# Kernel optimization log

Hardware: AMD Instinct MI355X
Metric: run time of the kernel (lower is better)

## Reference

```python
import jax, jax.numpy as jnp
import numpy as np

H = 2048          # hidden_size
NH = 32           # num_attention_heads
NKV = 8           # num_key_value_heads
HD = H // NH      # head_dim = 64
GROUPS = NH // NKV
B, S = 1, 4096


def setup_inputs() -> dict:
    key = jax.random.key(0)
    k1, k2, k3, k4, k5 = jax.random.split(key, 5)
    hidden_states = jax.random.normal(k1, (B, S, H), dtype=jnp.float32)
    # additive causal mask [B, 1, S, S]
    causal = jnp.tril(jnp.ones((S, S), dtype=bool))
    attention_mask = jnp.where(causal, 0.0, jnp.finfo(jnp.float32).min)[None, None].astype(jnp.float32)
    scale = 0.02
    Wq = jax.random.normal(k2, (H, H), dtype=jnp.float32) * scale
    Wk = jax.random.normal(k3, (NKV * HD, H), dtype=jnp.float32) * scale
    Wv = jax.random.normal(k4, (NKV * HD, H), dtype=jnp.float32) * scale
    Wo = jax.random.normal(k5, (H, H), dtype=jnp.float32) * scale
    return {"hidden_states": hidden_states, "attention_mask": attention_mask,
            "Wq": Wq, "Wk": Wk, "Wv": Wv, "Wo": Wo}


def reference(hidden_states, attention_mask, Wq, Wk, Wv, Wo):
    bsz, q_len, _ = hidden_states.shape
    # projections (nn.Linear: x @ W.T)
    q = (hidden_states @ Wq.T).reshape(bsz, q_len, NH, HD).transpose(0, 2, 1, 3)   # [B,NH,S,HD]
    k = (hidden_states @ Wk.T).reshape(bsz, q_len, NKV, HD).transpose(0, 2, 1, 3)  # [B,NKV,S,HD]
    v = (hidden_states @ Wv.T).reshape(bsz, q_len, NKV, HD).transpose(0, 2, 1, 3)
    # repeat_kv: expand each KV head GROUPS times
    k = jnp.repeat(k, GROUPS, axis=1)  # [B,NH,S,HD]
    v = jnp.repeat(v, GROUPS, axis=1)
    attn_weights = jnp.einsum('bhqd,bhkd->bhqk', q, k) / jnp.sqrt(jnp.float32(HD))
    attn_weights = attn_weights + attention_mask
    attn_weights = jax.nn.softmax(attn_weights.astype(jnp.float32), axis=-1).astype(q.dtype)
    attn_output = jnp.einsum('bhqk,bhkd->bhqd', attn_weights, v)
    attn_output = attn_output.transpose(0, 2, 1, 3).reshape(bsz, q_len, H)
    return attn_output @ Wo.T
```

## Files before the change

### kernel.cpp

```cpp
#include <hip/hip_runtime.h>
#include <stdint.h>

#define S_LEN  4096
#define HDIM   2048
#define NHEADS 32
#define NKVH   8
#define HDSZ   64
#define KVDIM  (NKVH * HDSZ)
#define QKN    (HDIM + KVDIM)

typedef __bf16 v8bf16 __attribute__((ext_vector_type(8)));
typedef short  v4s    __attribute__((ext_vector_type(4)));
typedef float  v4f32  __attribute__((ext_vector_type(4)));

__device__ __forceinline__ unsigned short f2bf(float f) {
    uint32_t u = __builtin_bit_cast(uint32_t, f);
    uint32_t r = (u + 0x7fffu + ((u >> 16) & 1u)) >> 16;
    return (unsigned short)r;
}

__device__ __forceinline__ uint32_t pack_bf16(float a, float b) {
#if __has_builtin(__builtin_amdgcn_cvt_pk_bf16_f32)
    auto r = __builtin_amdgcn_cvt_pk_bf16_f32(a, b);
    return __builtin_bit_cast(uint32_t, r);
#else
    uint32_t ua = __builtin_bit_cast(uint32_t, a) + 0x8000u;
    uint32_t ub = __builtin_bit_cast(uint32_t, b) + 0x8000u;
    return (ua >> 16) | (ub & 0xffff0000u);
#endif
}

__device__ __forceinline__ float fast_exp2(float x) {
#if __has_builtin(__builtin_amdgcn_exp2f)
    return __builtin_amdgcn_exp2f(x);
#else
    float r; asm("v_exp_f32 %0, %1" : "=v"(r) : "v"(x)); return r;
#endif
}

__device__ __forceinline__ void async_load16(const void* g, void* l) {
    __builtin_amdgcn_global_load_lds((const __attribute__((address_space(1))) void*)g,
                                     (__attribute__((address_space(3))) void*)l,
                                     16, 0, 0);
}

#define SEG0 2097152
#define SEG1 3145728
#define SEG2 3407872
#define SEG3 3670016
#define SEGT 4718592
__global__ void cvt_all(const float* __restrict__ x,  const float* __restrict__ wq,
                        const float* __restrict__ wk, const float* __restrict__ wv,
                        const float* __restrict__ wo,
                        ushort4* __restrict__ xb, ushort4* __restrict__ wqkb,
                        ushort4* __restrict__ wvb, ushort4* __restrict__ wob,
                        float qscale)
{
    int i = blockIdx.x * blockDim.x + threadIdx.x;
    if (i >= SEGT) return;
    const float4* src; ushort4* dst; float s = 1.0f; int loc;
    if (i < SEG0)      { src = (const float4*)x;  dst = xb;   loc = i; }
    else if (i < SEG1) { src = (const float4*)wq; dst = wqkb; loc = i - SEG0; s = qscale; }
    else if (i < SEG2) { src = (const float4*)wk; dst = wqkb + 1048576; loc = i - SEG1; }
    else if (i < SEG3) { src = (const float4*)wv; dst = wvb;  loc = i - SEG2; }
    else               { src = (const float4*)wo; dst = wob;  loc = i - SEG3; }
    float4 f = src[loc];
    uint2 o;
    o.x = pack_bf16(f.x * s, f.y * s);
    o.y = pack_bf16(f.z * s, f.w * s);
    dst[loc] = __builtin_bit_cast(ushort4, o);
}


#define STAGE_A(buf, kh, t)                                                       \
    do {                                                                          \
        async_load16(A + aBase + (size_t)(t) * 64 + (kh) * 32,                    \
                     &smem[(buf) * 16384 + (kh) * 8192 + ldsSt]);                 \
        async_load16(A + aBase + (size_t)128 * Kd + (size_t)(t) * 64 + (kh) * 32, \
                     &smem[(buf) * 16384 + (kh) * 8192 + ldsSt + 4096]);          \
    } while (0)
#define STAGE_B(buf, kh, t)                                                       \
    do {                                                                          \
        async_load16(Bp + bBase + (size_t)(t) * 64 + (kh) * 32,                   \
                     &smem[32768 + (buf) * 16384 + (kh) * 8192 + ldsSt]);         \
        async_load16(Bp + bBase + (size_t)128 * Kd + (size_t)(t) * 64 + (kh) * 32,\
                     &smem[32768 + (buf) * 16384 + (kh) * 8192 + ldsSt + 4096]);  \
    } while (0)

#define LOAD_AF(khoff)                                                            \
    do {                                                                          \
        _Pragma("unroll")                                                         \
        for (int mi = 0; mi < 8; ++mi)                                            \
            af[mi] = *(const v8bf16*)&smem[curA + (khoff) + aRd + mi * 512];      \
    } while (0)

#define MFMA_PAIR(khoff, NI)                                                      \
    do {                                                                          \
        v8bf16 _b0 = *(const v8bf16*)&smem[curB + (khoff) + bRd + (NI) * 512];    \
        v8bf16 _b1 = *(const v8bf16*)&smem[curB + (khoff) + bRd + (NI) * 512 + 512];\
        __builtin_amdgcn_s_setprio(1);                                            \
        _Pragma("unroll")                                                         \
        for (int mi = 0; mi < 8; ++mi) {                                          \
            acc[mi][(NI)]     = __builtin_amdgcn_mfma_f32_16x16x32_bf16(af[mi], _b0, acc[mi][(NI)], 0, 0, 0);     \
            acc[mi][(NI) + 1] = __builtin_amdgcn_mfma_f32_16x16x32_bf16(af[mi], _b1, acc[mi][(NI) + 1], 0, 0, 0); \
        }                                                                         \
        __builtin_amdgcn_s_setprio(0);                                            \
    } while (0)

#define FENCE_BAR()                                                               \
    do {                                                                          \
        __builtin_amdgcn_sched_barrier(0);                                        \
        __builtin_amdgcn_s_barrier();                                             \
        __builtin_amdgcn_sched_barrier(0);                                        \
    } while (0)

#define WAITV(N) asm volatile("s_waitcnt vmcnt(" #N ")" ::: "memory")

template<bool F32OUT>
__device__ __forceinline__ void gemm256_body(
    const unsigned short* __restrict__ A,
    const unsigned short* __restrict__ Bp,
    void* __restrict__ Cout, int Nn, int Kd, int m0, int n0,
    unsigned short* __restrict__ smem)
{
    const int tid  = threadIdx.x;
    const int wave = tid >> 6;
    const int lane = tid & 63;
    const int lrow = lane & 15;
    const int quad = lane >> 4;
    const int wm = (wave >> 2) * 128;
    const int wn = (wave & 3) * 64;

    const int lr   = lane >> 2;
    const int sg4  = (lane & 3) ^ ((lane >> 3) & 3);
    const size_t aBase = (size_t)(m0 + wave * 16 + lr) * Kd + sg4 * 8;
    const size_t bBase = (size_t)(n0 + wave * 16 + lr) * Kd + sg4 * 8;
    const int ldsSt = wave * 512;

    const int rg4 = (quad ^ ((lrow >> 1) & 3)) * 8;
    const int aRd = (wm + lrow) * 32 + rg4;
    const int bRd = (wn + lrow) * 32 + rg4;

    const int NT = Kd >> 6;

    v4f32 acc[8][4];
#pragma unroll
    for (int mi = 0; mi < 8; ++mi)
#pragma unroll
        for (int ni = 0; ni < 4; ++ni)
#pragma unroll
            for (int r = 0; r < 4; ++r) acc[mi][ni][r] = 0.0f;

    STAGE_A(0, 0, 0); STAGE_B(0, 0, 0);
    STAGE_A(0, 1, 0); STAGE_B(0, 1, 0);
    STAGE_A(1, 0, 1); STAGE_B(1, 0, 1);
    WAITV(8);
    __builtin_amdgcn_s_barrier();
    __builtin_amdgcn_sched_barrier(0);

    v8bf16 af[8];
    for (int t = 0; t < NT - 2; ++t) {
        const int cur  = t & 1;
        const int nxt  = cur ^ 1;
        const int curA = cur * 16384;
        const int curB = 32768 + cur * 16384;

        STAGE_A(nxt, 1, t + 1);
        LOAD_AF(0);
        MFMA_PAIR(0, 0);
        FENCE_BAR();

        STAGE_B(nxt, 1, t + 1);
        MFMA_PAIR(0, 2);
        WAITV(8);
        FENCE_BAR();

        STAGE_A(cur, 0, t + 2);
        LOAD_AF(8192);
        MFMA_PAIR(8192, 0);
        FENCE_BAR();

        STAGE_B(cur, 0, t + 2);
        MFMA_PAIR(8192, 2);
        WAITV(8);
        FENCE_BAR();
    }

    {
        const int t = NT - 2;
        const int cur  = t & 1;
        const int nxt  = cur ^ 1;
        const int curA = cur * 16384;
        const int curB = 32768 + cur * 16384;

        STAGE_A(nxt, 1, t + 1);
        LOAD_AF(0);
        MFMA_PAIR(0, 0);
        FENCE_BAR();

        STAGE_B(nxt, 1, t + 1);
        MFMA_PAIR(0, 2);
        WAITV(8);
        FENCE_BAR();

        LOAD_AF(8192);
        MFMA_PAIR(8192, 0);
        FENCE_BAR();

        MFMA_PAIR(8192, 2);
        WAITV(4);
        FENCE_BAR();
    }

    {
        const int cur  = (NT - 1) & 1;
        const int curA = cur * 16384;
        const int curB = 32768 + cur * 16384;

        LOAD_AF(0);
        MFMA_PAIR(0, 0);
        FENCE_BAR();

        MFMA_PAIR(0, 2);
        WAITV(0);
        FENCE_BAR();

        LOAD_AF(8192);
        MFMA_PAIR(8192, 0);
        FENCE_BAR();

        MFMA_PAIR(8192, 2);
    }

    if (F32OUT) {
        float* Cf = (float*)Cout;
#pragma unroll
        for (int mi = 0; mi < 8; ++mi)
#pragma unroll
            for (int ni = 0; ni < 4; ++ni)
#pragma unroll
                for (int r = 0; r < 4; ++r) {
                    const int row = m0 + wm + mi * 16 + quad * 4 + r;
                    const int col = n0 + wn + ni * 16 + lrow;
                    Cf[(size_t)row * Nn + col] = acc[mi][ni][r];
                }
    } else {
        unsigned short* Cb = (unsigned short*)Cout;
#pragma unroll
        for (int mi = 0; mi < 8; ++mi)
#pragma unroll
            for (int ni = 0; ni < 4; ++ni)
#pragma unroll
                for (int r = 0; r < 4; ++r) {
                    const int row = m0 + wm + mi * 16 + quad * 4 + r;
                    const int col = n0 + wn + ni * 16 + lrow;
                    Cb[(size_t)row * Nn + col] = f2bf(acc[mi][ni][r]);
                }
    }
}

__global__ __launch_bounds__(512, 2)
void gemm_qkv256(const unsigned short* __restrict__ xb,
                 const unsigned short* __restrict__ Wqkb,
                 const unsigned short* __restrict__ Wvb,
                 unsigned short* __restrict__ QKb,
                 unsigned short* __restrict__ Vtb)
{
    __shared__ __align__(16) unsigned short smem[65536];
    const int bid = blockIdx.x;
    if (bid < 32) {
        gemm256_body<false>(Wvb, xb, Vtb, S_LEN, HDIM,
                            (bid >> 4) * 256, (bid & 15) * 256, smem);
    } else {
        const int b = bid - 32;
        gemm256_body<false>(xb, Wqkb, QKb, QKN, HDIM,
                            (b & 15) * 256, (b >> 4) * 256, smem);
    }
}

__global__ __launch_bounds__(512, 2)
void gemm_o256(const unsigned short* __restrict__ A,
               const unsigned short* __restrict__ B,
               float* __restrict__ Cout)
{
    __shared__ __align__(16) unsigned short smem[65536];
    const int bid = blockIdx.x;
    gemm256_body<true>(A, B, Cout, HDIM, HDIM,
                       (bid & 15) * 256, (bid >> 4) * 256, smem);
}

__global__ __launch_bounds__(256, 3)
void flash_attn(const unsigned short* __restrict__ QK,
                const unsigned short* __restrict__ Vt,
                unsigned short* __restrict__ O)
{
    __shared__ unsigned short smem[24576];
    unsigned short* Qs = smem;

    const int tid  = threadIdx.x;
    const int wave = tid >> 6;
    const int lane = tid & 63;
    const int lrow = lane & 15;
    const int quad = lane >> 4;

    const int h   = blockIdx.x;
    const int kvh = h >> 2;
    const int q0  = (gridDim.y - 1 - blockIdx.y) * 128;

    const int srow8 = lane >> 3;
    const int sgrp  = (lane & 7) ^ srow8;
    const v8bf16 v_one8 = __builtin_bit_cast(v8bf16,
        (uint4){0x3F803F80u, 0x3F803F80u, 0x3F803F80u, 0x3F803F80u});

    {
        const size_t gq = (size_t)(q0 + wave * 32 + srow8) * QKN + h * HDSZ + sgrp * 8;
#pragma unroll
        for (int i = 0; i < 4; ++i)
            async_load16(QK + gq + (size_t)(i * 8) * QKN, &Qs[(wave * 32 + i * 8) * 64]);
    }

    int kperm[2];
#pragma unroll
    for (int i = 0; i < 2; ++i) {
        const int slot = wave * 16 + i * 8 + srow8;
        const int nj = slot >> 4, sm = slot & 15;
        kperm[i] = 32 * (nj >> 1) + 8 * (sm >> 2) + 4 * (nj & 1) + (sm & 3);
    }

    auto stage_kv = [&](int j) {
        const int k0b = j * 64;
        const int buf = (j & 1) * 4096;
#pragma unroll
        for (int i = 0; i < 2; ++i) {
            const size_t gk = (size_t)(k0b + kperm[i]) * QKN
                              + HDIM + kvh * HDSZ + sgrp * 8;
            async_load16(QK + gk, &smem[8192 + buf + (wave * 16 + i * 8) * 64]);
        }
        const size_t gv = (size_t)(kvh * HDSZ + wave * 16 + srow8) * S_LEN
                          + k0b + sgrp * 8;
        async_load16(Vt + gv,             &smem[16384 + buf + (wave * 16) * 64]);
        async_load16(Vt + gv + 8 * S_LEN, &smem[16384 + buf + (wave * 16 + 8) * 64]);
    };

    v4f32 o_acc[2][4], l_acc[2];
#pragma unroll
    for (int mi = 0; mi < 2; ++mi) {
#pragma unroll
        for (int r = 0; r < 4; ++r) l_acc[mi][r] = 0.0f;
#pragma unroll
        for (int dj = 0; dj < 4; ++dj)
#pragma unroll
            for (int r = 0; r < 4; ++r) o_acc[mi][dj][r] = 0.0f;
    }

    const int rbase = q0 + wave * 32;
    const int njt   = (q0 >> 6) + 2;

    stage_kv(0);

    for (int j = 0; j < njt; ++j) {
        const int k0  = j * 64;
        const int buf = (j & 1) * 4096;

        if (j + 1 < njt) { stage_kv(j + 1); WAITV(4); }
        else             { WAITV(0); }
        __builtin_amdgcn_sched_barrier(0);
        __builtin_amdgcn_s_barrier();
        __builtin_amdgcn_sched_barrier(0);

        if (k0 <= rbase + 31) {
            const unsigned short* Ks = &smem[8192 + buf];
            const unsigned short* Vs = &smem[16384 + buf];

            v4f32 st[2][4];
#pragma unroll
            for (int mi = 0; mi < 2; ++mi)
#pragma unroll
                for (int nj = 0; nj < 4; ++nj)
#pragma unroll
                    for (int r = 0; r < 4; ++r) st[mi][nj][r] = 0.0f;
#pragma unroll
            for (int kk = 0; kk < 2; ++kk) {
                const int swz = ((kk * 4 + quad) ^ (lrow & 7)) * 8;
                v8bf16 qa[2];
                qa[0] = *(const v8bf16*)&Qs[(wave * 32 + lrow) * 64 + swz];
                qa[1] = *(const v8bf16*)&Qs[(wave * 32 + 16 + lrow) * 64 + swz];
                __builtin_amdgcn_s_setprio(1);
#pragma unroll
                for (int nj = 0; nj < 4; ++nj) {
                    const v8bf16 kb = *(const v8bf16*)&Ks[(nj * 16 + lrow) * 64 + swz];
                    st[0][nj] = __builtin_amdgcn_mfma_f32_16x16x32_bf16(kb, qa[0], st[0][nj], 0, 0, 0);
                    st[1][nj] = __builtin_amdgcn_mfma_f32_16x16x32_bf16(kb, qa[1], st[1][nj], 0, 0, 0);
                }
                __builtin_amdgcn_s_setprio(0);
            }

            if (k0 + 63 > rbase) {
#pragma unroll
                for (int mi = 0; mi < 2; ++mi) {
                    const int qi = rbase + mi * 16 + lrow;
#pragma unroll
                    for (int nj = 0; nj < 4; ++nj) {
                        const int kib = k0 + 32 * (nj >> 1) + 8 * quad + 4 * (nj & 1);
#pragma unroll
                        for (int r = 0; r < 4; ++r)
                            if (kib + r > qi) st[mi][nj][r] = -1e30f;
                    }
                }
            }

            v8bf16 pk8[2][2];
#pragma unroll
            for (int mi = 0; mi < 2; ++mi) {
                uint2 pu[4];
#pragma unroll
                for (int nj = 0; nj < 4; ++nj) {
                    const float p0 = fast_exp2(st[mi][nj][0]);
                    const float p1 = fast_exp2(st[mi][nj][1]);
                    const float p2 = fast_exp2(st[mi][nj][2]);
                    const float p3 = fast_exp2(st[mi][nj][3]);
                    pu[nj].x = pack_bf16(p0, p1);
                    pu[nj].y = pack_bf16(p2, p3);
                }
                pk8[mi][0] = __builtin_bit_cast(v8bf16, (uint4){pu[0].x, pu[0].y, pu[1].x, pu[1].y});
                pk8[mi][1] = __builtin_bit_cast(v8bf16, (uint4){pu[2].x, pu[2].y, pu[3].x, pu[3].y});
            }

#pragma unroll
            for (int t = 0; t < 2; ++t) {
                const int swzv = ((t * 4 + quad) ^ (lrow & 7)) * 8;
                v8bf16 va[4];
#pragma unroll
                for (int dj = 0; dj < 4; ++dj)
                    va[dj] = *(const v8bf16*)&Vs[(dj * 16 + lrow) * 64 + swzv];
                __builtin_amdgcn_s_setprio(1);
#pragma unroll
                for (int dj = 0; dj < 4; ++dj) {
                    o_acc[0][dj] = __builtin_amdgcn_mfma_f32_16x16x32_bf16(va[dj], pk8[0][t], o_acc[0][dj], 0, 0, 0);
                    o_acc[1][dj] = __builtin_amdgcn_mfma_f32_16x16x32_bf16(va[dj], pk8[1][t], o_acc[1][dj], 0, 0, 0);
                }
                l_acc[0] = __builtin_amdgcn_mfma_f32_16x16x32_bf16(v_one8, pk8[0][t], l_acc[0], 0, 0, 0);
                l_acc[1] = __builtin_amdgcn_mfma_f32_16x16x32_bf16(v_one8, pk8[1][t], l_acc[1], 0, 0, 0);
                __builtin_amdgcn_s_setprio(0);
            }
        }

        __builtin_amdgcn_sched_barrier(0);
        __builtin_amdgcn_s_barrier();
        __builtin_amdgcn_sched_barrier(0);
    }

    __syncthreads();
    unsigned short* Os = smem;
#pragma unroll
    for (int mi = 0; mi < 2; ++mi) {
        const float inv = 1.0f / l_acc[mi][0];
#pragma unroll
        for (int dj = 0; dj < 4; ++dj)
#pragma unroll
            for (int r = 0; r < 4; ++r)
                Os[(wave * 32 + mi * 16 + lrow) * 72 + dj * 16 + quad * 4 + r] =
                    f2bf(o_acc[mi][dj][r] * inv);
    }
    __syncthreads();
#pragma unroll
    for (int i = 0; i < 4; ++i) {
        const int idx = i * 256 + tid;
        const int row = idx >> 3, c8 = idx & 7;
        const uint4 vv = *(const uint4*)&Os[row * 72 + c8 * 8];
        *(uint4*)&O[(size_t)(q0 + row) * HDIM + h * HDSZ + c8 * 8] = vv;
    }
}

extern "C" void kernel_launch(void* const* d_in, const int* in_sizes, int n_in,
                              void* d_out, int out_size, void* d_ws, size_t ws_size,
                              hipStream_t stream)
{
    const float* x  = (const float*)d_in[0];
    const float* Wq = (const float*)d_in[2];
    const float* Wk = (const float*)d_in[3];
    const float* Wv = (const float*)d_in[4];
    const float* Wo = (const float*)d_in[5];
    float* out = (float*)d_out;

    unsigned short* xb   = (unsigned short*)d_ws;
    unsigned short* Wqkb = xb   + (size_t)S_LEN * HDIM;
    unsigned short* Wvb  = Wqkb + (size_t)QKN * HDIM;
    unsigned short* Wob  = Wvb  + (size_t)KVDIM * HDIM;
    unsigned short* QKb  = Wob  + (size_t)HDIM * HDIM;
    unsigned short* Vtb  = QKb  + (size_t)S_LEN * QKN;
    unsigned short* AOb  = xb;

    cvt_all<<<(SEGT + 255) / 256, 256, 0, stream>>>(
        x, Wq, Wk, Wv, Wo,
        (ushort4*)xb, (ushort4*)Wqkb, (ushort4*)Wvb, (ushort4*)Wob,
        0.18033688011f);

    gemm_qkv256<<<192, 512, 0, stream>>>(xb, Wqkb, Wvb, QKb, Vtb);

    flash_attn<<<dim3(NHEADS, S_LEN / 128), 256, 0, stream>>>(QKb, Vtb, AOb);

    gemm_o256<<<128, 512, 0, stream>>>(AOb, Wob, out);
}
```

Baseline: 341.7 us.

## Replace O-projection GEMM with 128x256 tile kernel using deeper async pipeline

Swaps the generic 256x256 output-projection GEMM for a dedicated 128x256 tile kernel launched on 256 blocks instead of 128. The new kernel stages the K dimension in 32-wide half-tiles across double buffers, interleaving async global-to-LDS loads with MFMA pairs, and raises wave priority around the MFMAs. The aim is better CU coverage on MI355X, since 128 blocks leave many of its CUs idle, and better overlap of loads with compute. In exchange the tiles are smaller so data reuse per block drops, occupancy is limited to one block per CU, and the kernel carries hand-written prologue and epilogue code.

```diff
diff --git a/kernel.cpp b/kernel.cpp
--- a/kernel.cpp
+++ b/kernel.cpp
@@ -278,15 +278,166 @@
     }
 }
 
-__global__ __launch_bounds__(512, 2)
-void gemm_o256(const unsigned short* __restrict__ A,
-               const unsigned short* __restrict__ B,
+
+#define STAGE2_A(buf, kh, t)                                                      \
+    async_load16(A + aBase + (size_t)(t) * 64 + (kh) * 32,                        \
+                 &smem[(buf) * 8192 + (kh) * 4096 + ldsSt])
+#define STAGE2_B(buf, kh, t)                                                      \
+    do {                                                                          \
+        async_load16(Bp + bBase + (size_t)(t) * 64 + (kh) * 32,                   \
+                     &smem[16384 + (buf) * 16384 + (kh) * 8192 + ldsSt]);         \
+        async_load16(Bp + bBase + (size_t)128 * 2048 + (size_t)(t) * 64 + (kh) * 32,\
+                     &smem[16384 + (buf) * 16384 + (kh) * 8192 + ldsSt + 4096]);  \
+    } while (0)
+
+#define LOAD_AF2(khoff)                                                           \
+    do {                                                                          \
+        _Pragma("unroll")                                                         \
+        for (int mi = 0; mi < 4; ++mi)                                            \
+            af[mi] = *(const v8bf16*)&smem[curA + (khoff) + aRd + mi * 512];      \
+    } while (0)
+
+#define MFMA_PAIR2(khoff, NI)                                                     \
+    do {                                                                          \
+        v8bf16 _b0 = *(const v8bf16*)&smem[curB + (khoff) + bRd + (NI) * 512];    \
+        v8bf16 _b1 = *(const v8bf16*)&smem[curB + (khoff) + bRd + (NI) * 512 + 512];\
+        __builtin_amdgcn_s_setprio(1);                                            \
+        _Pragma("unroll")                                                         \
+        for (int mi = 0; mi < 4; ++mi) {                                          \
+            acc[mi][(NI)]     = __builtin_amdgcn_mfma_f32_16x16x32_bf16(af[mi], _b0, acc[mi][(NI)], 0, 0, 0);     \
+            acc[mi][(NI) + 1] = __builtin_amdgcn_mfma_f32_16x16x32_bf16(af[mi], _b1, acc[mi][(NI) + 1], 0, 0, 0); \
+        }                                                                         \
+        __builtin_amdgcn_s_setprio(0);                                            \
+    } while (0)
+
+__global__ __launch_bounds__(512, 1)
+void gemm_o128(const unsigned short* __restrict__ A,
+               const unsigned short* __restrict__ Bp,
                float* __restrict__ Cout)
 {
-    __shared__ __align__(16) unsigned short smem[65536];
-    const int bid = blockIdx.x;
-    gemm256_body<true>(A, B, Cout, HDIM, HDIM,
-                       (bid & 15) * 256, (bid >> 4) * 256, smem);
+    __shared__ __align__(16) unsigned short smem[49152];
+    const int tid  = threadIdx.x;
+    const int wave = tid >> 6;
+    const int lane = tid & 63;
+    const int lrow = lane & 15;
+    const int quad = lane >> 4;
+    const int wmi = wave >> 2;
+    const int wni = wave & 3;
+
+    const int m0 = (blockIdx.x >> 3) * 128;
+    const int n0 = (blockIdx.x & 7) * 256;
+
+    const int lr   = lane >> 2;
+    const int sg4  = (lane & 3) ^ ((lane >> 3) & 3);
+    const size_t aBase = (size_t)(m0 + wave * 16 + lr) * 2048 + sg4 * 8;
+    const size_t bBase = (size_t)(n0 + wave * 16 + lr) * 2048 + sg4 * 8;
+    const int ldsSt = wave * 512;
+
+    const int rg4 = (quad ^ ((lrow >> 1) & 3)) * 8;
+    const int aRd = (wmi * 64 + lrow) * 32 + rg4;
+    const int bRd = (wni * 64 + lrow) * 32 + rg4;
+
+    const int NT = 32;
+
+    v4f32 acc[4][4];
+#pragma unroll
+    for (int mi = 0; mi < 4; ++mi)
+#pragma unroll
+        for (int ni = 0; ni < 4; ++ni)
+#pragma unroll
+            for (int r = 0; r < 4; ++r) acc[mi][ni][r] = 0.0f;
+
+    STAGE2_A(0, 0, 0); STAGE2_B(0, 0, 0);
+    STAGE2_A(0, 1, 0); STAGE2_B(0, 1, 0);
+    STAGE2_A(1, 0, 1); STAGE2_B(1, 0, 1);
+    WAITV(6);
+    __builtin_amdgcn_s_barrier();
+    __builtin_amdgcn_sched_barrier(0);
+
+    v8bf16 af[4];
+    for (int t = 0; t < NT - 2; ++t) {
+        const int cur  = t & 1;
+        const int nxt  = cur ^ 1;
+        const int curA = cur * 8192;
+        const int curB = 16384 + cur * 16384;
+
+        STAGE2_A(nxt, 1, t + 1);
+        LOAD_AF2(0);
+        MFMA_PAIR2(0, 0);
+        FENCE_BAR();
+
+        STAGE2_B(nxt, 1, t + 1);
+        MFMA_PAIR2(0, 2);
+        WAITV(6);
+        FENCE_BAR();
+
+        STAGE2_A(cur, 0, t + 2);
+        LOAD_AF2(4096);
+        MFMA_PAIR2(8192, 0);
+        FENCE_BAR();
+
+        STAGE2_B(cur, 0, t + 2);
+        MFMA_PAIR2(8192, 2);
+        WAITV(6);
+        FENCE_BAR();
+    }
+
+    {
+        const int t = NT - 2;
+        const int cur  = t & 1;
+        const int nxt  = cur ^ 1;
+        const int curA = cur * 8192;
+        const int curB = 16384 + cur * 16384;
+
+        STAGE2_A(nxt, 1, t + 1);
+        LOAD_AF2(0);
+        MFMA_PAIR2(0, 0);
+        FENCE_BAR();
+
+        STAGE2_B(nxt, 1, t + 1);
+        MFMA_PAIR2(0, 2);
+        WAITV(6);
+        FENCE_BAR();
+
+        LOAD_AF2(4096);
+        MFMA_PAIR2(8192, 0);
+        FENCE_BAR();
+
+        MFMA_PAIR2(8192, 2);
+        WAITV(3);
+        FENCE_BAR();
+    }
+
+    {
+        const int cur  = (NT - 1) & 1;
+        const int curA = cur * 8192;
+        const int curB = 16384 + cur * 16384;
+
+        LOAD_AF2(0);
+        MFMA_PAIR2(0, 0);
+        FENCE_BAR();
+
+        MFMA_PAIR2(0, 2);
+        WAITV(0);
+        FENCE_BAR();
+
+        LOAD_AF2(4096);
+        MFMA_PAIR2(8192, 0);
+        FENCE_BAR();
+
+        MFMA_PAIR2(8192, 2);
+    }
+
+#pragma unroll
+    for (int mi = 0; mi < 4; ++mi)
+#pragma unroll
+        for (int ni = 0; ni < 4; ++ni)
+#pragma unroll
+            for (int r = 0; r < 4; ++r) {
+                const int row = m0 + wmi * 64 + mi * 16 + quad * 4 + r;
+                const int col = n0 + wni * 64 + ni * 16 + lrow;
+                Cout[(size_t)row * HDIM + col] = acc[mi][ni][r];
+            }
 }
 
 __global__ __launch_bounds__(256, 3)
@@ -500,5 +651,5 @@
 
     flash_attn<<<dim3(NHEADS, S_LEN / 128), 256, 0, stream>>>(QKb, Vtb, AOb);
 
-    gemm_o256<<<128, 512, 0, stream>>>(AOb, Wob, out);
-}
+    gemm_o128<<<256, 512, 0, stream>>>(AOb, Wob, out);
+}
```

Result: faster. 329.3 us (-3.6%).
